# Performance work log

Hardware: AMD Instinct MI355X
Metric: run time of the kernel (lower is better)

The kernel has to match this reference:

```python
import jax, jax.numpy as jnp
import numpy as np

B, C, H, W = 1, 448, 64, 64
K, M, PAD, STRIDE = 7, 7, 3, 1
CG = C // K          # key/query channels (KeyQueryMap divides by k) = 64
GP_HID = int(0.5 * CG)  # geometry prior hidden channels = 32
K2 = K * K
CENTER = K2 // 2


def conv1x1(x, w, b):
    # x: (B, Cin, H, W), w: (Cout, Cin), b: (Cout,)
    return jnp.einsum('bchw,oc->bohw', x, w) + b[None, :, None, None]


def unfold(x):
    # torch.nn.Unfold(K, dilation=1, padding=PAD, stride=STRIDE)
    # output layout: (B, Cin*K2, L) with dim1 index = c*K2 + (di*K + dj)
    Bc, Cc, Hc, Wc = x.shape
    xp = jnp.pad(x, ((0, 0), (0, 0), (PAD, PAD), (PAD, PAD)))
    Ho = (Hc + 2 * PAD - K) // STRIDE + 1
    Wo = (Wc + 2 * PAD - K) // STRIDE + 1
    patches = [xp[:, :, di:di + Ho * STRIDE:STRIDE, dj:dj + Wo * STRIDE:STRIDE]
               for di in range(K) for dj in range(K)]
    u = jnp.stack(patches, axis=2)  # (B, Cc, K2, Ho, Wo)
    return u.reshape(Bc, Cc * K2, Ho * Wo), Ho, Wo


def geometry_prior(gp_w1, gp_b1, gp_w2, gp_b2):
    ar = jnp.arange(-(K // 2), K // 2 + 1, dtype=jnp.float32)   # -3..3
    x_pos = jnp.broadcast_to(ar[None, :], (K, K))
    y_pos = jnp.broadcast_to(ar[::-1][:, None], (K, K))          # 3..-3 down rows
    pos = jnp.stack([x_pos, y_pos], axis=0)[None]                # (1, 2, K, K)
    h = jax.nn.relu(conv1x1(pos, gp_w1, gp_b1))
    out = conv1x1(h, gp_w2, gp_b2)                               # (1, CG, K, K)
    return out.reshape(1, CG, 1, K2)


def setup_inputs() -> dict:
    key = jax.random.key(0)
    ks = jax.random.split(key, 12)
    def lin(k, cout, cin):
        return jax.random.normal(k, (cout, cin), jnp.float32) / np.sqrt(cin)
    inp = {
        'x': jax.random.normal(ks[0], (B, C, H, W), jnp.float32),
        'Wk': lin(ks[1], CG, C), 'bk': jnp.zeros((CG,), jnp.float32),
        'Wq': lin(ks[2], CG, C), 'bq': jnp.zeros((CG,), jnp.float32),
        'gp_w1': lin(ks[3], GP_HID, 2), 'gp_b1': jax.random.normal(ks[4], (GP_HID,), jnp.float32) * 0.01,
        'gp_w2': lin(ks[5], CG, GP_HID), 'gp_b2': jax.random.normal(ks[6], (CG,), jnp.float32) * 0.01,
        'Wf': lin(ks[7], C, C), 'bf': jnp.zeros((C,), jnp.float32),
    }
    return inp


def reference(x, Wk, bk, Wq, bq, gp_w1, gp_b1, gp_w2, gp_b2, Wf, bf):
    gpk = geometry_prior(gp_w1, gp_b1, gp_w2, gp_b2)        # (1, CG, 1, K2)
    km = conv1x1(x, Wk, bk)                                  # (B, CG, H, W)
    qm = conv1x1(x, Wq, bq)
    ku, Ho, Wo = unfold(km)
    L = Ho * Wo
    ku = ku.reshape(B, CG, L, K2)   # same row-major semantics as torch .view
    qu, _, _ = unfold(qm)
    qu = qu.reshape(B, CG, L, K2)
    ak = ku * qu[:, :, :, CENTER:CENTER + 1]                 # (B, CG, L, K2)
    ck = jax.nn.softmax(ak + gpk, axis=-1)                   # (B, CG, L, K2)
    xu, _, _ = unfold(x)
    xu = xu.reshape(B, M, C // M, L, K2)                     # (B, M, CG, L, K2)
    # ck broadcasts over the M axis (valid since B == 1); sum over window dim
    pre = jnp.einsum('bglp,bmglp->bmgl', ck, xu).reshape(B, C, Ho, Wo)
    return conv1x1(pre, Wf, bf)
```

## Files before the change

### kernel.cpp

```cpp
#include <hip/hip_runtime.h>
#include <hip/hip_bf16.h>

#define CC   448
#define CGC  64
#define MMM  7
#define HWSZ 4096
#define KK2  49
#define GPH  32

typedef __attribute__((ext_vector_type(8))) short   short8;
typedef __attribute__((ext_vector_type(4))) float   f32x4;
typedef __attribute__((ext_vector_type(4))) unsigned short us4;

__device__ __forceinline__ unsigned short f2b(float f) {
    union { __hip_bfloat16 h; unsigned short u; } cv;
    cv.h = __float2bfloat16(f);
    return cv.u;
}

__device__ __forceinline__ void mfma_gemm64(
    const float* __restrict__ A,
    const float* __restrict__ B,
    const float* __restrict__ bias,
    float* __restrict__ C,
    int nT, int tid)
{
    __shared__ unsigned short As[2048];
    __shared__ unsigned short Bs[2048];
    __shared__ float bias_s[64];
    if (tid < 64) bias_s[tid] = bias[tid];

    const int lane = tid & 63;
    const int wid  = tid >> 6;
    const int wm   = (wid >> 1) * 32;
    const int wn   = (wid & 1) * 32;
    const int l15  = lane & 15;
    const int l4   = lane >> 4;

    const int am0 = tid >> 3,          ak0 = tid & 7;
    const int am1 = (tid + 256) >> 3,  ak1 = (tid + 256) & 7;
    const int bk0 = tid >> 4,          bn0 = tid & 15;
    const int bk1 = (tid + 256) >> 4,  bn1 = (tid + 256) & 15;

    f32x4 acc[2][2];
    #pragma unroll
    for (int i = 0; i < 2; ++i)
        #pragma unroll
        for (int j = 0; j < 2; ++j)
            acc[i][j] = (f32x4){0.f, 0.f, 0.f, 0.f};

    float4 a0 = *(const float4*)(A + am0 * CC + ak0 * 4);
    float4 a1 = *(const float4*)(A + am1 * CC + ak1 * 4);
    float4 b0 = *(const float4*)(B + (size_t)bk0 * HWSZ + nT + bn0 * 4);
    float4 b1 = *(const float4*)(B + (size_t)bk1 * HWSZ + nT + bn1 * 4);

    for (int kt = 0; kt < 14; ++kt) {
        {
            us4 w0 = { f2b(a0.x), f2b(a0.y), f2b(a0.z), f2b(a0.w) };
            *(us4*)&As[(ak0 >> 1) * 512 + am0 * 8 + (ak0 & 1) * 4] = w0;
            us4 w1 = { f2b(a1.x), f2b(a1.y), f2b(a1.z), f2b(a1.w) };
            *(us4*)&As[(ak1 >> 1) * 512 + am1 * 8 + (ak1 & 1) * 4] = w1;
            int base0 = (bk0 >> 3) * 512 + bn0 * 32 + (bk0 & 7);
            Bs[base0]      = f2b(b0.x);
            Bs[base0 + 8]  = f2b(b0.y);
            Bs[base0 + 16] = f2b(b0.z);
            Bs[base0 + 24] = f2b(b0.w);
            int base1 = (bk1 >> 3) * 512 + bn1 * 32 + (bk1 & 7);
            Bs[base1]      = f2b(b1.x);
            Bs[base1 + 8]  = f2b(b1.y);
            Bs[base1 + 16] = f2b(b1.z);
            Bs[base1 + 24] = f2b(b1.w);
        }
        if (kt < 13) {
            int ko = (kt + 1) * 32;
            a0 = *(const float4*)(A + am0 * CC + ko + ak0 * 4);
            a1 = *(const float4*)(A + am1 * CC + ko + ak1 * 4);
            b0 = *(const float4*)(B + (size_t)(ko + bk0) * HWSZ + nT + bn0 * 4);
            b1 = *(const float4*)(B + (size_t)(ko + bk1) * HWSZ + nT + bn1 * 4);
        }
        __syncthreads();
        short8 fa0 = *(short8*)&As[l4 * 512 + (wm + l15) * 8];
        short8 fa1 = *(short8*)&As[l4 * 512 + (wm + 16 + l15) * 8];
        short8 fb0 = *(short8*)&Bs[l4 * 512 + (wn + l15) * 8];
        short8 fb1 = *(short8*)&Bs[l4 * 512 + (wn + 16 + l15) * 8];
        acc[0][0] = __builtin_amdgcn_mfma_f32_16x16x32_bf16(fa0, fb0, acc[0][0], 0, 0, 0);
        acc[0][1] = __builtin_amdgcn_mfma_f32_16x16x32_bf16(fa0, fb1, acc[0][1], 0, 0, 0);
        acc[1][0] = __builtin_amdgcn_mfma_f32_16x16x32_bf16(fa1, fb0, acc[1][0], 0, 0, 0);
        acc[1][1] = __builtin_amdgcn_mfma_f32_16x16x32_bf16(fa1, fb1, acc[1][1], 0, 0, 0);
        __syncthreads();
    }
    #pragma unroll
    for (int wm2 = 0; wm2 < 2; ++wm2)
        #pragma unroll
        for (int wn2 = 0; wn2 < 2; ++wn2)
            #pragma unroll
            for (int r = 0; r < 4; ++r) {
                int row = wm + wm2 * 16 + l4 * 4 + r;
                int col = wn + wn2 * 16 + l15;
                C[(size_t)row * HWSZ + nT + col] = acc[wm2][wn2][r] + bias_s[row];
            }
}

__global__ __launch_bounds__(256) void kq_mfma(
    const float* __restrict__ x,
    const float* __restrict__ Wk, const float* __restrict__ bk,
    const float* __restrict__ Wq, const float* __restrict__ bq,
    float* __restrict__ km, float* __restrict__ qm)
{
    const bool isQ = (blockIdx.y != 0);
    mfma_gemm64(isQ ? Wq : Wk, x, isQ ? bq : bk, isQ ? qm : km,
                blockIdx.x * 64, threadIdx.x);
}

__global__ __launch_bounds__(256) void fconv_mfma(
    const float* __restrict__ pre,
    const float* __restrict__ Wf, const float* __restrict__ bfv,
    float* __restrict__ out)
{
    const int mt = blockIdx.y;
    mfma_gemm64(Wf + (size_t)mt * 64 * CC, pre, bfv + mt * 64,
                out + (size_t)mt * 64 * HWSZ, blockIdx.x * 64, threadIdx.x);
}

#define GLO 196
#define GHI 260
#define XWORDS (GLO + HWSZ + GHI)

__device__ __forceinline__ int win_off_global(int n, bool& ok) {
    int p  = n >> 12;
    int l  = n & 4095;
    int di = (p * 37) >> 8;
    int dj = p - di * 7;
    int i  = (l >> 6) + di - 3;
    int j  = (l & 63) + dj - 3;
    ok = ((unsigned)i < 64u) && ((unsigned)j < 64u);
    return i * 64 + j;
}

__global__ __launch_bounds__(256) void attn_kernel(
    const float* __restrict__ km, const float* __restrict__ qm,
    const float* __restrict__ x,
    const float* __restrict__ gw1, const float* __restrict__ gb1,
    const float* __restrict__ gw2, const float* __restrict__ gb2,
    float* __restrict__ pre)
{
    __shared__ float klin[XWORDS];
    __shared__ float xlin[XWORDS];
    __shared__ float gpk_s[KK2];
    const int tid = threadIdx.x;
    const int g   = blockIdx.y;
    const int lp  = blockIdx.x * 256 + tid;

    if (tid < 114) {
        float4 z = {0.f, 0.f, 0.f, 0.f};
        int w = (tid < 49) ? tid * 4 : (GLO + HWSZ + (tid - 49) * 4);
        *(float4*)&klin[w] = z;
        *(float4*)&xlin[w] = z;
    }
    {
        const float4* km4 = (const float4*)(km + (size_t)g * HWSZ);
        #pragma unroll
        for (int i = 0; i < 4; ++i) {
            int idx = tid + i * 256;
            *(float4*)&klin[GLO + idx * 4] = km4[idx];
        }
    }
    if (tid < KK2) {
        int di = tid / 7, dj = tid - di * 7;
        float xp = (float)(dj - 3);
        float yp = (float)(3 - di);
        float acc = gb2[g];
        #pragma unroll
        for (int j = 0; j < GPH; ++j) {
            float h = gw1[j * 2 + 0] * xp + gw1[j * 2 + 1] * yp + gb1[j];
            h = fmaxf(h, 0.f);
            acc = fmaf(gw2[g * GPH + j], h, acc);
        }
        gpk_s[tid] = acc;
    }

    float qc;
    { bool ok; int o = win_off_global(lp * KK2 + 24, ok); qc = ok ? qm[(size_t)g * HWSZ + o] : 0.f; }

    const int n0 = lp * KK2;
    const int p0 = n0 >> 12;
    const int l0 = n0 & 4095;
    const int ts = ((p0 + 1) << 12) - n0;
    const int di0 = (p0 * 37) >> 8, dj0 = p0 - di0 * 7;
    const int p1  = p0 + 1;
    const int di1 = (p1 * 37) >> 8, dj1 = p1 - di1 * 7;
    const int djm3_0 = dj0 - 3, djm3_1 = dj1 - 3;
    const int B0 = GLO + l0 + (di0 - 3) * 64 + djm3_0;
    const int B1 = GLO + l0 - 4096 + (di1 - 3) * 64 + djm3_1;

    float4 xr0, xr1, xr2, xr3;
    {
        const float4* xg4 = (const float4*)(x + (size_t)g * HWSZ);
        xr0 = xg4[tid]; xr1 = xg4[tid + 256]; xr2 = xg4[tid + 512]; xr3 = xg4[tid + 768];
    }
    __syncthreads();

    float a[KK2];
    float mx = -1e30f;
    #pragma unroll
    for (int t = 0; t < KK2; ++t) {
        bool s1 = (t >= ts);
        int base = s1 ? B1 : B0;
        float kv = klin[base + t];
        int jj = ((l0 + t) & 63) + (s1 ? djm3_1 : djm3_0);
        kv = ((unsigned)jj < 64u) ? kv : 0.f;
        float av = fmaf(kv, qc, gpk_s[t]);
        a[t] = av;
        mx = fmaxf(mx, av);
    }
    float d = 0.f;
    #pragma unroll
    for (int t = 0; t < KK2; ++t) {
        float e = __expf(a[t] - mx);
        d += e;
        bool s1 = (t >= ts);
        int jj = ((l0 + t) & 63) + (s1 ? djm3_1 : djm3_0);
        a[t] = ((unsigned)jj < 64u) ? e : 0.f;
    }
    const float inv = 1.f / d;

    #pragma unroll 1
    for (int m = 0; m < MMM; ++m) {
        __syncthreads();
        *(float4*)&xlin[GLO + tid * 4]          = xr0;
        *(float4*)&xlin[GLO + (tid + 256) * 4]  = xr1;
        *(float4*)&xlin[GLO + (tid + 512) * 4]  = xr2;
        *(float4*)&xlin[GLO + (tid + 768) * 4]  = xr3;
        if (m < MMM - 1) {
            const float4* xg4 = (const float4*)(x + (size_t)((m + 1) * CGC + g) * HWSZ);
            xr0 = xg4[tid]; xr1 = xg4[tid + 256]; xr2 = xg4[tid + 512]; xr3 = xg4[tid + 768];
        }
        __syncthreads();
        float acc = 0.f;
        #pragma unroll
        for (int t = 0; t < KK2; ++t) {
            int base = (t >= ts) ? B1 : B0;
            acc = fmaf(a[t], xlin[base + t], acc);
        }
        pre[(size_t)(m * CGC + g) * HWSZ + lp] = acc * inv;
    }
}

extern "C" void kernel_launch(void* const* d_in, const int* in_sizes, int n_in,
                              void* d_out, int out_size, void* d_ws, size_t ws_size,
                              hipStream_t stream) {
    const float* x   = (const float*)d_in[0];
    const float* Wk  = (const float*)d_in[1];
    const float* bk  = (const float*)d_in[2];
    const float* Wq  = (const float*)d_in[3];
    const float* bq  = (const float*)d_in[4];
    const float* gw1 = (const float*)d_in[5];
    const float* gb1 = (const float*)d_in[6];
    const float* gw2 = (const float*)d_in[7];
    const float* gb2 = (const float*)d_in[8];
    const float* Wf  = (const float*)d_in[9];
    const float* bfv = (const float*)d_in[10];
    float* out = (float*)d_out;

    float* km  = (float*)d_ws;
    float* qm  = km + CGC * HWSZ;
    float* pre = qm + CGC * HWSZ;

    kq_mfma    <<<dim3(64, 2),  256, 0, stream>>>(x, Wk, bk, Wq, bq, km, qm);
    attn_kernel<<<dim3(16, CGC), 256, 0, stream>>>(km, qm, x, gw1, gb1, gw2, gb2, pre);
    fconv_mfma <<<dim3(64, 7),  256, 0, stream>>>(pre, Wf, bfv, out);
}
```

Measured before the change: 118.8 us.

## Fuse K/Q projections into one GEMM and halve N tiles for both GEMMs

The K and Q 1x1 convs now run as a single 128-row GEMM per 32-column tile, so x is loaded and converted once and shared by both projections. Each block writes its top half to km and its bottom half to qm. The final conv also drops to 32-column tiles, doubling the block count to improve occupancy across CUs. Smaller N tiles mean less reuse of the weight tile per block, so Wf and Wk/Wq are reloaded and converted more often.

```diff
diff --git a/kernel.cpp b/kernel.cpp
--- a/kernel.cpp
+++ b/kernel.cpp
@@ -18,98 +18,92 @@
     return cv.u;
 }
 
-__device__ __forceinline__ void mfma_gemm64(
-    const float* __restrict__ A,
-    const float* __restrict__ B,
-    const float* __restrict__ bias,
-    float* __restrict__ C,
-    int nT, int tid)
-{
-    __shared__ unsigned short As[2048];
-    __shared__ unsigned short Bs[2048];
-    __shared__ float bias_s[64];
-    if (tid < 64) bias_s[tid] = bias[tid];
-
-    const int lane = tid & 63;
-    const int wid  = tid >> 6;
-    const int wm   = (wid >> 1) * 32;
-    const int wn   = (wid & 1) * 32;
-    const int l15  = lane & 15;
-    const int l4   = lane >> 4;
-
-    const int am0 = tid >> 3,          ak0 = tid & 7;
-    const int am1 = (tid + 256) >> 3,  ak1 = (tid + 256) & 7;
-    const int bk0 = tid >> 4,          bn0 = tid & 15;
-    const int bk1 = (tid + 256) >> 4,  bn1 = (tid + 256) & 15;
-
-    f32x4 acc[2][2];
-    #pragma unroll
-    for (int i = 0; i < 2; ++i)
-        #pragma unroll
-        for (int j = 0; j < 2; ++j)
-            acc[i][j] = (f32x4){0.f, 0.f, 0.f, 0.f};
-
-    float4 a0 = *(const float4*)(A + am0 * CC + ak0 * 4);
-    float4 a1 = *(const float4*)(A + am1 * CC + ak1 * 4);
-    float4 b0 = *(const float4*)(B + (size_t)bk0 * HWSZ + nT + bn0 * 4);
-    float4 b1 = *(const float4*)(B + (size_t)bk1 * HWSZ + nT + bn1 * 4);
-
-    for (int kt = 0; kt < 14; ++kt) {
-        {
-            us4 w0 = { f2b(a0.x), f2b(a0.y), f2b(a0.z), f2b(a0.w) };
-            *(us4*)&As[(ak0 >> 1) * 512 + am0 * 8 + (ak0 & 1) * 4] = w0;
-            us4 w1 = { f2b(a1.x), f2b(a1.y), f2b(a1.z), f2b(a1.w) };
-            *(us4*)&As[(ak1 >> 1) * 512 + am1 * 8 + (ak1 & 1) * 4] = w1;
-            int base0 = (bk0 >> 3) * 512 + bn0 * 32 + (bk0 & 7);
-            Bs[base0]      = f2b(b0.x);
-            Bs[base0 + 8]  = f2b(b0.y);
-            Bs[base0 + 16] = f2b(b0.z);
-            Bs[base0 + 24] = f2b(b0.w);
-            int base1 = (bk1 >> 3) * 512 + bn1 * 32 + (bk1 & 7);
-            Bs[base1]      = f2b(b1.x);
-            Bs[base1 + 8]  = f2b(b1.y);
-            Bs[base1 + 16] = f2b(b1.z);
-            Bs[base1 + 24] = f2b(b1.w);
-        }
-        if (kt < 13) {
-            int ko = (kt + 1) * 32;
-            a0 = *(const float4*)(A + am0 * CC + ko + ak0 * 4);
-            a1 = *(const float4*)(A + am1 * CC + ko + ak1 * 4);
-            b0 = *(const float4*)(B + (size_t)(ko + bk0) * HWSZ + nT + bn0 * 4);
-            b1 = *(const float4*)(B + (size_t)(ko + bk1) * HWSZ + nT + bn1 * 4);
-        }
-        __syncthreads();
-        short8 fa0 = *(short8*)&As[l4 * 512 + (wm + l15) * 8];
-        short8 fa1 = *(short8*)&As[l4 * 512 + (wm + 16 + l15) * 8];
-        short8 fb0 = *(short8*)&Bs[l4 * 512 + (wn + l15) * 8];
-        short8 fb1 = *(short8*)&Bs[l4 * 512 + (wn + 16 + l15) * 8];
-        acc[0][0] = __builtin_amdgcn_mfma_f32_16x16x32_bf16(fa0, fb0, acc[0][0], 0, 0, 0);
-        acc[0][1] = __builtin_amdgcn_mfma_f32_16x16x32_bf16(fa0, fb1, acc[0][1], 0, 0, 0);
-        acc[1][0] = __builtin_amdgcn_mfma_f32_16x16x32_bf16(fa1, fb0, acc[1][0], 0, 0, 0);
-        acc[1][1] = __builtin_amdgcn_mfma_f32_16x16x32_bf16(fa1, fb1, acc[1][1], 0, 0, 0);
-        __syncthreads();
-    }
-    #pragma unroll
-    for (int wm2 = 0; wm2 < 2; ++wm2)
-        #pragma unroll
-        for (int wn2 = 0; wn2 < 2; ++wn2)
-            #pragma unroll
-            for (int r = 0; r < 4; ++r) {
-                int row = wm + wm2 * 16 + l4 * 4 + r;
-                int col = wn + wn2 * 16 + l15;
-                C[(size_t)row * HWSZ + nT + col] = acc[wm2][wn2][r] + bias_s[row];
-            }
-}
-
 __global__ __launch_bounds__(256) void kq_mfma(
     const float* __restrict__ x,
     const float* __restrict__ Wk, const float* __restrict__ bk,
     const float* __restrict__ Wq, const float* __restrict__ bq,
     float* __restrict__ km, float* __restrict__ qm)
 {
-    const bool isQ = (blockIdx.y != 0);
-    mfma_gemm64(isQ ? Wq : Wk, x, isQ ? bq : bk, isQ ? qm : km,
-                blockIdx.x * 64, threadIdx.x);
+    __shared__ unsigned short As[4096];
+    __shared__ unsigned short Bs[1024];
+
+    const int tid  = threadIdx.x;
+    const int nT   = blockIdx.x * 32;
+    const int lane = tid & 63;
+    const int wid  = tid >> 6;
+    const int wm   = wid * 32;
+    const int l15  = lane & 15;
+    const int l4   = lane >> 4;
+
+    const int ar = tid >> 3;
+    const int ak = tid & 7;
+    const int bkr = tid >> 3;
+    const int bn4 = tid & 7;
+
+    f32x4 acc[2][2];
+    #pragma unroll
+    for (int i = 0; i < 2; ++i)
+        #pragma unroll
+        for (int j = 0; j < 2; ++j)
+            acc[i][j] = (f32x4){0.f, 0.f, 0.f, 0.f};
+
+    float4 a0 = *(const float4*)(Wk + (size_t)ar * CC + ak * 4);
+    float4 a1 = *(const float4*)(Wk + (size_t)(ar + 32) * CC + ak * 4);
+    float4 a2 = *(const float4*)(Wq + (size_t)ar * CC + ak * 4);
+    float4 a3 = *(const float4*)(Wq + (size_t)(ar + 32) * CC + ak * 4);
+    float4 b0 = *(const float4*)(x + (size_t)bkr * HWSZ + nT + bn4 * 4);
+
+    for (int kt = 0; kt < 14; ++kt) {
+        {
+            int kg = ak >> 1, jo = (ak & 1) * 4;
+            us4 w;
+            w = (us4){ f2b(a0.x), f2b(a0.y), f2b(a0.z), f2b(a0.w) };
+            *(us4*)&As[kg * 1024 + (ar +  0) * 8 + jo] = w;
+            w = (us4){ f2b(a1.x), f2b(a1.y), f2b(a1.z), f2b(a1.w) };
+            *(us4*)&As[kg * 1024 + (ar + 32) * 8 + jo] = w;
+            w = (us4){ f2b(a2.x), f2b(a2.y), f2b(a2.z), f2b(a2.w) };
+            *(us4*)&As[kg * 1024 + (ar + 64) * 8 + jo] = w;
+            w = (us4){ f2b(a3.x), f2b(a3.y), f2b(a3.z), f2b(a3.w) };
+            *(us4*)&As[kg * 1024 + (ar + 96) * 8 + jo] = w;
+            int base = (bkr >> 3) * 256 + bn4 * 32 + (bkr & 7);
+            Bs[base]      = f2b(b0.x);
+            Bs[base + 8]  = f2b(b0.y);
+            Bs[base + 16] = f2b(b0.z);
+            Bs[base + 24] = f2b(b0.w);
+        }
+        if (kt < 13) {
+            int ko = (kt + 1) * 32;
+            a0 = *(const float4*)(Wk + (size_t)ar * CC + ko + ak * 4);
+            a1 = *(const float4*)(Wk + (size_t)(ar + 32) * CC + ko + ak * 4);
+            a2 = *(const float4*)(Wq + (size_t)ar * CC + ko + ak * 4);
+            a3 = *(const float4*)(Wq + (size_t)(ar + 32) * CC + ko + ak * 4);
+            b0 = *(const float4*)(x + (size_t)(ko + bkr) * HWSZ + nT + bn4 * 4);
+        }
+        __syncthreads();
+        short8 fa0 = *(short8*)&As[l4 * 1024 + (wm + l15) * 8];
+        short8 fa1 = *(short8*)&As[l4 * 1024 + (wm + 16 + l15) * 8];
+        short8 fb0 = *(short8*)&Bs[l4 * 256 + l15 * 8];
+        short8 fb1 = *(short8*)&Bs[l4 * 256 + (16 + l15) * 8];
+        acc[0][0] = __builtin_amdgcn_mfma_f32_16x16x32_bf16(fa0, fb0, acc[0][0], 0, 0, 0);
+        acc[0][1] = __builtin_amdgcn_mfma_f32_16x16x32_bf16(fa0, fb1, acc[0][1], 0, 0, 0);
+        acc[1][0] = __builtin_amdgcn_mfma_f32_16x16x32_bf16(fa1, fb0, acc[1][0], 0, 0, 0);
+        acc[1][1] = __builtin_amdgcn_mfma_f32_16x16x32_bf16(fa1, fb1, acc[1][1], 0, 0, 0);
+        __syncthreads();
+    }
+    const bool isK = (wid < 2);
+    float*       Cd   = isK ? km : qm;
+    const float* bias = isK ? bk : bq;
+    const int rbase = (wm & 63);
+    #pragma unroll
+    for (int wm2 = 0; wm2 < 2; ++wm2)
+        #pragma unroll
+        for (int wn2 = 0; wn2 < 2; ++wn2)
+            #pragma unroll
+            for (int r = 0; r < 4; ++r) {
+                int row = rbase + wm2 * 16 + l4 * 4 + r;
+                int col = nT + wn2 * 16 + l15;
+                Cd[(size_t)row * HWSZ + col] = acc[wm2][wn2][r] + bias[row];
+            }
 }
 
 __global__ __launch_bounds__(256) void fconv_mfma(
@@ -117,9 +111,68 @@
     const float* __restrict__ Wf, const float* __restrict__ bfv,
     float* __restrict__ out)
 {
-    const int mt = blockIdx.y;
-    mfma_gemm64(Wf + (size_t)mt * 64 * CC, pre, bfv + mt * 64,
-                out + (size_t)mt * 64 * HWSZ, blockIdx.x * 64, threadIdx.x);
+    __shared__ unsigned short As[2048];
+    __shared__ unsigned short Bs[1024];
+
+    const int tid  = threadIdx.x;
+    const int nT   = blockIdx.x * 32;
+    const int oT   = blockIdx.y * 64;
+    const int lane = tid & 63;
+    const int wid  = tid >> 6;
+    const int l15  = lane & 15;
+    const int l4   = lane >> 4;
+
+    const int ar = tid >> 3;
+    const int ak = tid & 7;
+    const int bkr = tid >> 3;
+    const int bn4 = tid & 7;
+
+    const float* __restrict__ A = Wf + (size_t)oT * CC;
+
+    f32x4 acc[2];
+    acc[0] = (f32x4){0.f, 0.f, 0.f, 0.f};
+    acc[1] = (f32x4){0.f, 0.f, 0.f, 0.f};
+
+    float4 a0 = *(const float4*)(A + (size_t)ar * CC + ak * 4);
+    float4 a1 = *(const float4*)(A + (size_t)(ar + 32) * CC + ak * 4);
+    float4 b0 = *(const float4*)(pre + (size_t)bkr * HWSZ + nT + bn4 * 4);
+
+    for (int kt = 0; kt < 14; ++kt) {
+        {
+            int kg = ak >> 1, jo = (ak & 1) * 4;
+            us4 w;
+            w = (us4){ f2b(a0.x), f2b(a0.y), f2b(a0.z), f2b(a0.w) };
+            *(us4*)&As[kg * 512 + (ar +  0) * 8 + jo] = w;
+            w = (us4){ f2b(a1.x), f2b(a1.y), f2b(a1.z), f2b(a1.w) };
+            *(us4*)&As[kg * 512 + (ar + 32) * 8 + jo] = w;
+            int base = (bkr >> 3) * 256 + bn4 * 32 + (bkr & 7);
+            Bs[base]      = f2b(b0.x);
+            Bs[base + 8]  = f2b(b0.y);
+            Bs[base + 16] = f2b(b0.z);
+            Bs[base + 24] = f2b(b0.w);
+        }
+        if (kt < 13) {
+            int ko = (kt + 1) * 32;
+            a0 = *(const float4*)(A + (size_t)ar * CC + ko + ak * 4);
+            a1 = *(const float4*)(A + (size_t)(ar + 32) * CC + ko + ak * 4);
+            b0 = *(const float4*)(pre + (size_t)(ko + bkr) * HWSZ + nT + bn4 * 4);
+        }
+        __syncthreads();
+        short8 fa  = *(short8*)&As[l4 * 512 + (wid * 16 + l15) * 8];
+        short8 fb0 = *(short8*)&Bs[l4 * 256 + l15 * 8];
+        short8 fb1 = *(short8*)&Bs[l4 * 256 + (16 + l15) * 8];
+        acc[0] = __builtin_amdgcn_mfma_f32_16x16x32_bf16(fa, fb0, acc[0], 0, 0, 0);
+        acc[1] = __builtin_amdgcn_mfma_f32_16x16x32_bf16(fa, fb1, acc[1], 0, 0, 0);
+        __syncthreads();
+    }
+    #pragma unroll
+    for (int wn2 = 0; wn2 < 2; ++wn2)
+        #pragma unroll
+        for (int r = 0; r < 4; ++r) {
+            int row = oT + wid * 16 + l4 * 4 + r;
+            int col = nT + wn2 * 16 + l15;
+            out[(size_t)row * HWSZ + col] = acc[wn2][r] + bfv[row];
+        }
 }
 
 #define GLO 196
@@ -266,7 +319,7 @@
     float* qm  = km + CGC * HWSZ;
     float* pre = qm + CGC * HWSZ;
 
-    kq_mfma    <<<dim3(64, 2),  256, 0, stream>>>(x, Wk, bk, Wq, bq, km, qm);
+    kq_mfma    <<<dim3(128),     256, 0, stream>>>(x, Wk, bk, Wq, bq, km, qm);
     attn_kernel<<<dim3(16, CGC), 256, 0, stream>>>(km, qm, x, gw1, gb1, gw2, gb2, pre);
-    fconv_mfma <<<dim3(64, 7),  256, 0, stream>>>(pre, Wf, bfv, out);
-}
+    fconv_mfma <<<dim3(128, 7),  256, 0, stream>>>(pre, Wf, bfv, out);
+}
```

Measured after the change: 115.9 us. -2.5%, faster.
